# Optimization experiments

Hardware: AMD Instinct MI355X
Metric: run time of the kernel (lower is better)

## Reference

```python
import jax, jax.numpy as jnp
import numpy as np

D_MODEL = 1024
N_HEADS = 16
D_K = D_MODEL // N_HEADS


def setup_inputs() -> dict:
    key = jax.random.key(0)
    kx, kq, kk, kv, ko = jax.random.split(key, 5)
    s = 1.0 / np.sqrt(D_MODEL)
    return {
        "x": jax.random.normal(kx, (4, 2048, D_MODEL), dtype=jnp.float32),
        "W_q": jax.random.normal(kq, (D_MODEL, D_MODEL), dtype=jnp.float32) * s,
        "W_k": jax.random.normal(kk, (D_MODEL, D_MODEL), dtype=jnp.float32) * s,
        "W_v": jax.random.normal(kv, (D_MODEL, D_MODEL), dtype=jnp.float32) * s,
        "W_o": jax.random.normal(ko, (D_MODEL, D_MODEL), dtype=jnp.float32) * s,
    }


def reference(x, W_q, W_k, W_v, W_o):
    B, S, _ = x.shape
    # torch nn.Linear computes x @ W.T; our W_* stored as [out, in]-equivalent square,
    # use plain x @ W (equivalent parameterization for a random weight).
    def split_heads(t):  # [B,S,D] -> [B,H,S,d_k]
        return t.reshape(B, S, N_HEADS, D_K).transpose(0, 2, 1, 3)

    Q = split_heads(x @ W_q)
    K = split_heads(x @ W_k)
    V = split_heads(x @ W_v)
    scale = 1.0 / np.sqrt(D_K).astype(np.float32)
    scores = jnp.einsum('bhqd,bhkd->bhqk', Q, K) * scale  # [B,H,S,S]
    causal_mask = jnp.tril(jnp.ones((S, S), dtype=bool))  # True = keep
    scores = jnp.where(causal_mask, scores, jnp.float32(-jnp.inf))
    attn = jax.nn.softmax(scores, axis=-1)
    out = jnp.einsum('bhqk,bhkd->bhqd', attn, V)  # [B,H,S,d_k]
    out = out.transpose(0, 2, 1, 3).reshape(B, S, D_MODEL)
    return out @ W_o
```

## Files before the change

kernel.cpp:

```cpp
#include <hip/hip_runtime.h>
#include <hip/hip_bf16.h>
#include <stdint.h>

#define B_SZ 4
#define SEQ 2048
#define DM 1024
#define NH 16
#define DK 64
#define BH (B_SZ * NH)
#define M_TOT (B_SZ * SEQ)

typedef unsigned short u16;
typedef u16 u16x8 __attribute__((ext_vector_type(8)));
typedef __bf16 bf16x8 __attribute__((ext_vector_type(8)));
typedef float f32x4 __attribute__((ext_vector_type(4)));

__device__ __forceinline__ u16 f2bf(float f) {
    union { float f; uint32_t u; } v; v.f = f;
    uint32_t u = v.u;
    return (u16)((u + 0x7FFFu + ((u >> 16) & 1u)) >> 16);
}

__device__ __forceinline__ f32x4 mfma16(u16x8 a, u16x8 b, f32x4 c) {
    return __builtin_amdgcn_mfma_f32_16x16x32_bf16(
        __builtin_bit_cast(bf16x8, a), __builtin_bit_cast(bf16x8, b), c, 0, 0, 0);
}

__device__ __forceinline__ void gload16_lds(const void* g, void* l) {
    __builtin_amdgcn_global_load_lds(
        (const __attribute__((address_space(1))) void*)(uintptr_t)g,
        (__attribute__((address_space(3))) void*)(uintptr_t)l, 16, 0, 0);
}

__global__ void cvt_bf16_kernel(const float* __restrict__ in, u16* __restrict__ out, int n4) {
    int i = blockIdx.x * blockDim.x + threadIdx.x;
    if (i < n4) {
        float4 v = ((const float4*)in)[i];
        ushort4 o;
        o.x = f2bf(v.x); o.y = f2bf(v.y); o.z = f2bf(v.z); o.w = f2bf(v.w);
        ((ushort4*)out)[i] = o;
    }
}

__global__ void transpose_w_kernel(const float* __restrict__ W0, const float* __restrict__ W1,
                                   u16* __restrict__ Wt) {
    __shared__ u16 tile[32][33];
    int bx = blockIdx.x, by = blockIdx.y, z = blockIdx.z;
    const float* W = z ? W1 : W0;
    u16* Wd = Wt + (size_t)z * DM * DM;
    int t = threadIdx.x;
    for (int i = 0; i < 4; i++) {
        int idx = t + i * 256;
        int r = idx >> 5, c = idx & 31;
        tile[r][c] = f2bf(W[(by * 32 + r) * DM + bx * 32 + c]);
    }
    __syncthreads();
    for (int i = 0; i < 4; i++) {
        int idx = t + i * 256;
        int r2 = idx >> 5, c2 = idx & 31;
        Wd[(bx * 32 + r2) * DM + by * 32 + c2] = tile[c2][r2];
    }
}

__global__ void vtrans_kernel(const u16* __restrict__ V, u16* __restrict__ Vt) {
    __shared__ u16 t[64][66];
    int s0 = blockIdx.x * 64, bh = blockIdx.y;
    int tid = threadIdx.x, lane = tid & 63, wave = tid >> 6;
    const u16* Vg = V + (size_t)bh * SEQ * DK;
    u16* Og = Vt + (size_t)bh * DK * SEQ;
    for (int i = 0; i < 2; i++) {
        int s = lane;
        int dc = wave + 4 * i;
        u16x8 v = *(const u16x8*)(&Vg[(size_t)(s0 + s) * DK + dc * 8]);
        for (int j = 0; j < 8; j++) t[dc * 8 + j][s] = v[j];
    }
    __syncthreads();
    int d = tid >> 2, ch = tid & 3;
    u16 tmp[16];
    for (int j = 0; j < 16; j++) tmp[j] = t[d][ch * 16 + j];
    *(uint4*)(&Og[(size_t)d * SEQ + s0 + ch * 16]) = *(uint4*)(&tmp[0]);
    *(uint4*)(&Og[(size_t)d * SEQ + s0 + ch * 16 + 8]) = *(uint4*)(&tmp[8]);
}

template <int AFP32, int MODE>
__global__ __launch_bounds__(256, 2) void gemm128(
    const void* __restrict__ Ain, const u16* __restrict__ Bt,
    void* __restrict__ C0p, void* __restrict__ C1p, float scale0) {
    __shared__ u16 As[128][32];
    __shared__ u16 Bs[128][32];
    const int K = DM;
    int m0 = blockIdx.x * 128;
    int n0 = blockIdx.y * 128;
    int tid = threadIdx.x;
    int lane = tid & 63, wave = tid >> 6;
    int quad = lane >> 4, l15 = lane & 15;
    int wm = wave >> 1, wn = wave & 1;

    f32x4 acc[4][4];
    for (int i = 0; i < 4; i++)
        for (int j = 0; j < 4; j++) acc[i][j] = f32x4{0.f, 0.f, 0.f, 0.f};

    int rS = lane >> 2;
    int cS = (lane & 3) * 8;

    for (int k0 = 0; k0 < K; k0 += 32) {
        __syncthreads();
        if (AFP32) {
            const float* A = (const float*)Ain;
            for (int i = 0; i < 4; i++) {
                int idx = tid + i * 256;
                int r = idx >> 3, c = (idx & 7) * 4;
                float4 v = *(const float4*)(&A[(size_t)(m0 + r) * K + k0 + c]);
                ushort4 o;
                o.x = f2bf(v.x); o.y = f2bf(v.y); o.z = f2bf(v.z); o.w = f2bf(v.w);
                *(ushort4*)(&As[r][c]) = o;
            }
        } else {
            const u16* A = (const u16*)Ain;
            const u16* ga = &A[(size_t)(m0 + wave * 32 + rS) * K + k0 + cS];
            gload16_lds(ga, &As[wave * 32][0]);
            gload16_lds(ga + (size_t)16 * K, &As[wave * 32 + 16][0]);
        }
        {
            const u16* gb = &Bt[(size_t)(n0 + wave * 32 + rS) * K + k0 + cS];
            gload16_lds(gb, &Bs[wave * 32][0]);
            gload16_lds(gb + (size_t)16 * K, &Bs[wave * 32 + 16][0]);
        }
        __syncthreads();
        u16x8 af[4], bfv[4];
        for (int mt = 0; mt < 4; mt++)
            af[mt] = *(const u16x8*)(&As[wm * 64 + mt * 16 + l15][quad * 8]);
        for (int nt = 0; nt < 4; nt++)
            bfv[nt] = *(const u16x8*)(&Bs[wn * 64 + nt * 16 + l15][quad * 8]);
        for (int mt = 0; mt < 4; mt++)
            for (int nt = 0; nt < 4; nt++)
                acc[mt][nt] = mfma16(af[mt], bfv[nt], acc[mt][nt]);
    }

    for (int mt = 0; mt < 4; mt++)
        for (int nt = 0; nt < 4; nt++)
            for (int r = 0; r < 4; r++) {
                int m = m0 + wm * 64 + mt * 16 + quad * 4 + r;
                int n = n0 + wn * 64 + nt * 16 + l15;
                float v = acc[mt][nt][r];
                if (MODE == 0) {
                    v *= (n < 1024) ? scale0 : 1.0f;
                    u16* C = (n < 1024) ? (u16*)C0p : (u16*)C1p;
                    int ne = n & 1023;
                    int b = m >> 11, s = m & 2047;
                    int h = ne >> 6, d = ne & 63;
                    C[(((size_t)(b * NH + h) * SEQ) + s) * DK + d] = f2bf(v);
                } else {
                    ((float*)C0p)[(size_t)m * DM + n] = v;
                }
            }
}

__global__ __launch_bounds__(128, 3) void attn_kernel(
    const u16* __restrict__ Qb, const u16* __restrict__ Kb,
    const u16* __restrict__ Vtb, u16* __restrict__ AOb) {
    __shared__ u16 Kl[2][64][32];
    __shared__ u16 Vl[2][64][32];
    __shared__ u16 Pl[64][72];

    int bh = blockIdx.x;
    int p = blockIdx.y;
    int tid = threadIdx.x, lane = tid & 63, wave = tid >> 6;
    int quad = lane >> 4, l15 = lane & 15;
    int b = bh >> 4, h = bh & 15;

    const u16* Qg = Qb + (size_t)bh * SEQ * DK;
    const u16* Kg = Kb + (size_t)bh * SEQ * DK;
    const u16* Vg = Vtb + (size_t)bh * DK * SEQ;

    int rS = lane >> 2;
    int cS = (lane & 3) * 8;
    u16* Pw = &Pl[wave * 32][0];

    for (int ph = 0; ph < 2; ph++) {
        int qs = ph ? (31 - p) : p;
        int q0 = qs * 64;

        u16x8 aq[2][2];
        for (int m = 0; m < 2; m++)
            for (int kc = 0; kc < 2; kc++)
                aq[m][kc] = *(const u16x8*)(
                    &Qg[(size_t)(q0 + wave * 32 + m * 16 + l15) * DK + kc * 32 + quad * 8]);

        float lsum[2][4];
        f32x4 O[2][4];
        for (int m = 0; m < 2; m++)
            for (int r = 0; r < 4; r++) lsum[m][r] = 0.f;
        for (int m = 0; m < 2; m++)
            for (int nt = 0; nt < 4; nt++) O[m][nt] = f32x4{0.f, 0.f, 0.f, 0.f};

        for (int kt = 0; kt <= qs; kt++) {
            int k0 = kt * 64;
            __syncthreads();
            {
                const u16* gk = &Kg[(size_t)(k0 + wave * 32 + rS) * DK + cS];
                gload16_lds(gk, &Kl[0][wave * 32][0]);
                gload16_lds(gk + (size_t)16 * DK, &Kl[0][wave * 32 + 16][0]);
                gload16_lds(gk + 32, &Kl[1][wave * 32][0]);
                gload16_lds(gk + (size_t)16 * DK + 32, &Kl[1][wave * 32 + 16][0]);
                const u16* gv = &Vg[(size_t)(wave * 32 + rS) * SEQ + k0 + cS];
                gload16_lds(gv, &Vl[0][wave * 32][0]);
                gload16_lds(gv + (size_t)16 * SEQ, &Vl[0][wave * 32 + 16][0]);
                gload16_lds(gv + 32, &Vl[1][wave * 32][0]);
                gload16_lds(gv + (size_t)16 * SEQ + 32, &Vl[1][wave * 32 + 16][0]);
            }
            __syncthreads();

            f32x4 sc[2][4];
            for (int nt = 0; nt < 4; nt++) {
                u16x8 b0 = *(const u16x8*)(&Kl[0][nt * 16 + l15][quad * 8]);
                u16x8 b1 = *(const u16x8*)(&Kl[1][nt * 16 + l15][quad * 8]);
                for (int m = 0; m < 2; m++) {
                    f32x4 z = f32x4{0.f, 0.f, 0.f, 0.f};
                    z = mfma16(aq[m][0], b0, z);
                    z = mfma16(aq[m][1], b1, z);
                    sc[m][nt] = z;
                }
            }
            if (kt == qs) {
                for (int m = 0; m < 2; m++)
                    for (int nt = 0; nt < 4; nt++)
                        for (int r = 0; r < 4; r++) {
                            int qq = wave * 32 + m * 16 + quad * 4 + r;
                            int kk = nt * 16 + l15;
                            float e = exp2f(sc[m][nt][r]);
                            float pv = (kk <= qq) ? e : 0.f;
                            sc[m][nt][r] = pv;
                            lsum[m][r] += pv;
                        }
            } else {
                for (int m = 0; m < 2; m++)
                    for (int nt = 0; nt < 4; nt++)
                        for (int r = 0; r < 4; r++) {
                            float pv = exp2f(sc[m][nt][r]);
                            sc[m][nt][r] = pv;
                            lsum[m][r] += pv;
                        }
            }
            for (int m = 0; m < 2; m++)
                for (int nt = 0; nt < 4; nt++)
                    for (int r = 0; r < 4; r++)
                        Pw[(size_t)(m * 16 + quad * 4 + r) * 72 + nt * 16 + l15] =
                            f2bf(sc[m][nt][r]);
            u16x8 ap[2][2];
            for (int m = 0; m < 2; m++)
                for (int kc = 0; kc < 2; kc++)
                    ap[m][kc] = *(const u16x8*)(
                        &Pw[(size_t)(m * 16 + l15) * 72 + kc * 32 + quad * 8]);
            for (int nt = 0; nt < 4; nt++) {
                u16x8 b0 = *(const u16x8*)(&Vl[0][nt * 16 + l15][quad * 8]);
                u16x8 b1 = *(const u16x8*)(&Vl[1][nt * 16 + l15][quad * 8]);
                for (int m = 0; m < 2; m++) {
                    O[m][nt] = mfma16(ap[m][0], b0, O[m][nt]);
                    O[m][nt] = mfma16(ap[m][1], b1, O[m][nt]);
                }
            }
        }

        for (int m = 0; m < 2; m++)
            for (int r = 0; r < 4; r++) {
                float s = lsum[m][r];
                for (int off = 1; off < 16; off <<= 1) s += __shfl_xor(s, off, 64);
                float inv = 1.0f / s;
                int q = q0 + wave * 32 + m * 16 + quad * 4 + r;
                for (int nt = 0; nt < 4; nt++) {
                    int d = nt * 16 + l15;
                    AOb[((size_t)(b * SEQ + q)) * DM + h * DK + d] = f2bf(O[m][nt][r] * inv);
                }
            }
    }
}

extern "C" void kernel_launch(void* const* d_in, const int* in_sizes, int n_in,
                              void* d_out, int out_size, void* d_ws, size_t ws_size,
                              hipStream_t stream) {
    const float* x = (const float*)d_in[0];
    const float* Wq = (const float*)d_in[1];
    const float* Wk = (const float*)d_in[2];
    const float* Wv = (const float*)d_in[3];
    const float* Wo = (const float*)d_in[4];

    const size_t HALF = (size_t)M_TOT * DM * 2;
    char* S0 = (char*)d_ws;
    char* S1 = (char*)d_ws + HALF;
    char* D0 = (char*)d_out;
    char* D1 = (char*)d_out + HALF;

    u16* xb   = (u16*)S0;
    u16* Qb   = (u16*)S1;
    u16* Kb   = (u16*)D1;
    u16* Vb   = (u16*)D0;
    u16* Vt   = (u16*)S0;
    u16* AOb  = (u16*)D0;
    u16* wqk  = (u16*)D0;
    u16* wvt  = (u16*)S0;
    u16* wot  = (u16*)D1;
    float* Cf = (float*)d_ws;

    const float cscale = 0.125f * 1.44269504088896f;
    dim3 tg2(32, 32, 2);
    dim3 tg1(32, 32, 1);

    int n4 = M_TOT * DM / 4;
    cvt_bf16_kernel<<<n4 / 256, 256, 0, stream>>>(x, xb, n4);

    transpose_w_kernel<<<tg2, 256, 0, stream>>>(Wq, Wk, wqk);
    dim3 gqk(M_TOT / 128, 2048 / 128);
    gemm128<0, 0><<<gqk, 256, 0, stream>>>(xb, wqk, (void*)Qb, (void*)Kb, cscale);

    transpose_w_kernel<<<tg1, 256, 0, stream>>>(Wv, Wv, wvt);
    dim3 gg(M_TOT / 128, DM / 128);
    gemm128<1, 0><<<gg, 256, 0, stream>>>(x, wvt, (void*)Vb, (void*)Vb, 1.0f);

    dim3 vg(SEQ / 64, BH);
    vtrans_kernel<<<vg, 256, 0, stream>>>(Vb, Vt);

    dim3 ag(BH, 16);
    attn_kernel<<<ag, 128, 0, stream>>>(Qb, Kb, Vt, AOb);

    transpose_w_kernel<<<tg1, 256, 0, stream>>>(Wo, Wo, wot);
    gemm128<0, 1><<<gg, 256, 0, stream>>>(AOb, wot, (void*)Cf, (void*)Cf, 1.0f);

    hipMemcpyAsync(d_out, d_ws, 2 * HALF, hipMemcpyDeviceToDevice, stream);
}
```

Baseline: 311.7 us.

## Split attention query tile across four waves and truncate P to bf16

```diff
diff --git a/kernel.cpp b/kernel.cpp
--- a/kernel.cpp
+++ b/kernel.cpp
@@ -19,6 +19,11 @@
     union { float f; uint32_t u; } v; v.f = f;
     uint32_t u = v.u;
     return (u16)((u + 0x7FFFu + ((u >> 16) & 1u)) >> 16);
+}
+
+__device__ __forceinline__ u16 f2bf_trunc(float f) {
+    union { float f; uint32_t u; } v; v.f = f;
+    return (u16)(v.u >> 16);
 }
 
 __device__ __forceinline__ f32x4 mfma16(u16x8 a, u16x8 b, f32x4 c) {
@@ -156,7 +161,7 @@
             }
 }
 
-__global__ __launch_bounds__(128, 3) void attn_kernel(
+__global__ __launch_bounds__(256, 4) void attn_kernel(
     const u16* __restrict__ Qb, const u16* __restrict__ Kb,
     const u16* __restrict__ Vtb, u16* __restrict__ AOb) {
     __shared__ u16 Kl[2][64][32];
@@ -175,104 +180,85 @@
 
     int rS = lane >> 2;
     int cS = (lane & 3) * 8;
-    u16* Pw = &Pl[wave * 32][0];
+    u16* Pw = &Pl[wave * 16][0];
 
     for (int ph = 0; ph < 2; ph++) {
         int qs = ph ? (31 - p) : p;
         int q0 = qs * 64;
 
-        u16x8 aq[2][2];
-        for (int m = 0; m < 2; m++)
-            for (int kc = 0; kc < 2; kc++)
-                aq[m][kc] = *(const u16x8*)(
-                    &Qg[(size_t)(q0 + wave * 32 + m * 16 + l15) * DK + kc * 32 + quad * 8]);
-
-        float lsum[2][4];
-        f32x4 O[2][4];
-        for (int m = 0; m < 2; m++)
-            for (int r = 0; r < 4; r++) lsum[m][r] = 0.f;
-        for (int m = 0; m < 2; m++)
-            for (int nt = 0; nt < 4; nt++) O[m][nt] = f32x4{0.f, 0.f, 0.f, 0.f};
+        u16x8 aq[2];
+        for (int kc = 0; kc < 2; kc++)
+            aq[kc] = *(const u16x8*)(
+                &Qg[(size_t)(q0 + wave * 16 + l15) * DK + kc * 32 + quad * 8]);
+
+        float lsum[4];
+        f32x4 O[4];
+        for (int r = 0; r < 4; r++) lsum[r] = 0.f;
+        for (int nt = 0; nt < 4; nt++) O[nt] = f32x4{0.f, 0.f, 0.f, 0.f};
 
         for (int kt = 0; kt <= qs; kt++) {
             int k0 = kt * 64;
             __syncthreads();
             {
-                const u16* gk = &Kg[(size_t)(k0 + wave * 32 + rS) * DK + cS];
-                gload16_lds(gk, &Kl[0][wave * 32][0]);
-                gload16_lds(gk + (size_t)16 * DK, &Kl[0][wave * 32 + 16][0]);
-                gload16_lds(gk + 32, &Kl[1][wave * 32][0]);
-                gload16_lds(gk + (size_t)16 * DK + 32, &Kl[1][wave * 32 + 16][0]);
-                const u16* gv = &Vg[(size_t)(wave * 32 + rS) * SEQ + k0 + cS];
-                gload16_lds(gv, &Vl[0][wave * 32][0]);
-                gload16_lds(gv + (size_t)16 * SEQ, &Vl[0][wave * 32 + 16][0]);
-                gload16_lds(gv + 32, &Vl[1][wave * 32][0]);
-                gload16_lds(gv + (size_t)16 * SEQ + 32, &Vl[1][wave * 32 + 16][0]);
+                const u16* gk = &Kg[(size_t)(k0 + wave * 16 + rS) * DK + cS];
+                gload16_lds(gk, &Kl[0][wave * 16][0]);
+                gload16_lds(gk + 32, &Kl[1][wave * 16][0]);
+                const u16* gv = &Vg[(size_t)(wave * 16 + rS) * SEQ + k0 + cS];
+                gload16_lds(gv, &Vl[0][wave * 16][0]);
+                gload16_lds(gv + 32, &Vl[1][wave * 16][0]);
             }
             __syncthreads();
 
-            f32x4 sc[2][4];
+            f32x4 sc[4];
             for (int nt = 0; nt < 4; nt++) {
                 u16x8 b0 = *(const u16x8*)(&Kl[0][nt * 16 + l15][quad * 8]);
                 u16x8 b1 = *(const u16x8*)(&Kl[1][nt * 16 + l15][quad * 8]);
-                for (int m = 0; m < 2; m++) {
-                    f32x4 z = f32x4{0.f, 0.f, 0.f, 0.f};
-                    z = mfma16(aq[m][0], b0, z);
-                    z = mfma16(aq[m][1], b1, z);
-                    sc[m][nt] = z;
-                }
+                f32x4 z = f32x4{0.f, 0.f, 0.f, 0.f};
+                z = mfma16(aq[0], b0, z);
+                z = mfma16(aq[1], b1, z);
+                sc[nt] = z;
             }
             if (kt == qs) {
-                for (int m = 0; m < 2; m++)
-                    for (int nt = 0; nt < 4; nt++)
-                        for (int r = 0; r < 4; r++) {
-                            int qq = wave * 32 + m * 16 + quad * 4 + r;
-                            int kk = nt * 16 + l15;
-                            float e = exp2f(sc[m][nt][r]);
-                            float pv = (kk <= qq) ? e : 0.f;
-                            sc[m][nt][r] = pv;
-                            lsum[m][r] += pv;
-                        }
+                for (int nt = 0; nt < 4; nt++)
+                    for (int r = 0; r < 4; r++) {
+                        int qq = wave * 16 + quad * 4 + r;
+                        int kk = nt * 16 + l15;
+                        float e = exp2f(sc[nt][r]);
+                        float pv = (kk <= qq) ? e : 0.f;
+                        sc[nt][r] = pv;
+                        lsum[r] += pv;
+                    }
             } else {
-                for (int m = 0; m < 2; m++)
-                    for (int nt = 0; nt < 4; nt++)
-                        for (int r = 0; r < 4; r++) {
-                            float pv = exp2f(sc[m][nt][r]);
-                            sc[m][nt][r] = pv;
-                            lsum[m][r] += pv;
-                        }
-            }
-            for (int m = 0; m < 2; m++)
                 for (int nt = 0; nt < 4; nt++)
-                    for (int r = 0; r < 4; r++)
-                        Pw[(size_t)(m * 16 + quad * 4 + r) * 72 + nt * 16 + l15] =
-                            f2bf(sc[m][nt][r]);
-            u16x8 ap[2][2];
-            for (int m = 0; m < 2; m++)
-                for (int kc = 0; kc < 2; kc++)
-                    ap[m][kc] = *(const u16x8*)(
-                        &Pw[(size_t)(m * 16 + l15) * 72 + kc * 32 + quad * 8]);
+                    for (int r = 0; r < 4; r++) {
+                        float pv = exp2f(sc[nt][r]);
+                        sc[nt][r] = pv;
+                        lsum[r] += pv;
+                    }
+            }
+            for (int nt = 0; nt < 4; nt++)
+                for (int r = 0; r < 4; r++)
+                    Pw[(size_t)(quad * 4 + r) * 72 + nt * 16 + l15] = f2bf_trunc(sc[nt][r]);
+            u16x8 ap0 = *(const u16x8*)(&Pw[(size_t)l15 * 72 + quad * 8]);
+            u16x8 ap1 = *(const u16x8*)(&Pw[(size_t)l15 * 72 + 32 + quad * 8]);
             for (int nt = 0; nt < 4; nt++) {
                 u16x8 b0 = *(const u16x8*)(&Vl[0][nt * 16 + l15][quad * 8]);
                 u16x8 b1 = *(const u16x8*)(&Vl[1][nt * 16 + l15][quad * 8]);
-                for (int m = 0; m < 2; m++) {
-                    O[m][nt] = mfma16(ap[m][0], b0, O[m][nt]);
-                    O[m][nt] = mfma16(ap[m][1], b1, O[m][nt]);
-                }
+                O[nt] = mfma16(ap0, b0, O[nt]);
+                O[nt] = mfma16(ap1, b1, O[nt]);
             }
         }
 
-        for (int m = 0; m < 2; m++)
-            for (int r = 0; r < 4; r++) {
-                float s = lsum[m][r];
-                for (int off = 1; off < 16; off <<= 1) s += __shfl_xor(s, off, 64);
-                float inv = 1.0f / s;
-                int q = q0 + wave * 32 + m * 16 + quad * 4 + r;
-                for (int nt = 0; nt < 4; nt++) {
-                    int d = nt * 16 + l15;
-                    AOb[((size_t)(b * SEQ + q)) * DM + h * DK + d] = f2bf(O[m][nt][r] * inv);
-                }
-            }
+        for (int r = 0; r < 4; r++) {
+            float s = lsum[r];
+            for (int off = 1; off < 16; off <<= 1) s += __shfl_xor(s, off, 64);
+            float inv = 1.0f / s;
+            int q = q0 + wave * 16 + quad * 4 + r;
+            for (int nt = 0; nt < 4; nt++) {
+                int d = nt * 16 + l15;
+                AOb[((size_t)(b * SEQ + q)) * DM + h * DK + d] = f2bf(O[nt][r] * inv);
+            }
+        }
     }
 }
 
@@ -321,7 +307,7 @@
     vtrans_kernel<<<vg, 256, 0, stream>>>(Vb, Vt);
 
     dim3 ag(BH, 16);
-    attn_kernel<<<ag, 128, 0, stream>>>(Qb, Kb, Vt, AOb);
+    attn_kernel<<<ag, 256, 0, stream>>>(Qb, Kb, Vt, AOb);
 
     transpose_w_kernel<<<tg1, 256, 0, stream>>>(Wo, Wo, wot);
     gemm128<0, 1><<<gg, 256, 0, stream>>>(AOb, wot, (void*)Cf, (void*)Cf, 1.0f);
```

Result: faster. 296.8 us (-4.8%).
